# Kernel tuning notes

Measured on AMD Instinct MI355X. Metric: run time of the kernel, lower is better.

The kernel has to match this reference:

```python
import jax, jax.numpy as jnp
import numpy as np
import math

B, L, D, H = 4, 4096, 1024, 16
d = D // H

def setup_inputs() -> dict:
    key = jax.random.key(0)
    ks = jax.random.split(key, 8)
    s = 0.02
    x = jax.random.normal(ks[0], (B, L, D), dtype=jnp.float32)
    Wqkv_w = jax.random.normal(ks[1], (3 * D, D), dtype=jnp.float32) * s
    Wqkv_b = jnp.zeros((3 * D,), dtype=jnp.float32)
    out_w = jax.random.normal(ks[2], (D, D), dtype=jnp.float32) * s
    out_b = jnp.zeros((D,), dtype=jnp.float32)
    W_static = jax.random.normal(ks[3], (H, d, d), dtype=jnp.float32) * s
    Lambda_raw = jax.random.uniform(ks[4], (H, d, d), dtype=jnp.float32, minval=-3.0, maxval=3.0)
    g = 0.5 / math.sqrt(d)
    Gamma = jax.random.uniform(ks[5], (H, d, d), dtype=jnp.float32, minval=-g, maxval=g)
    return {"x": x, "Wqkv_w": Wqkv_w, "Wqkv_b": Wqkv_b, "out_w": out_w,
            "out_b": out_b, "W_static": W_static, "Lambda_raw": Lambda_raw, "Gamma": Gamma}

def _stp_forward(x, Wqkv_w, Wqkv_b, out_w, out_b, W_static, Lambda_raw, Gamma):
    b, l, dm = x.shape
    scale = 1.0 / math.sqrt(d)
    qkv = x @ Wqkv_w.T + Wqkv_b                      # (B,L,3D)
    qkv = qkv.reshape(b, l, 3, H, d)                 # 'b l (three h d)'
    qkv = jnp.transpose(qkv, (2, 0, 3, 1, 4))        # (3,B,H,L,d)
    q, k, v = qkv[0], qkv[1], qkv[2]
    k = k * scale
    retention = 1.0 - jax.nn.sigmoid(Lambda_raw)     # (H,d,d)

    # scan over time: carry state (B,H,d,d)
    qs = jnp.moveaxis(q, 2, 0)                       # (L,B,H,d)
    ks_ = jnp.moveaxis(k, 2, 0)
    vs = jnp.moveaxis(v, 2, 0)

    def step(state, qkv_t):
        q_t, k_t, v_t = qkv_t                        # each (B,H,d)
        hebbian = jnp.einsum('bhi,bhj->bhij', v_t, k_t)
        state = retention[None] * state + Gamma[None] * hebbian
        y_t = jnp.einsum('bhij,bhj->bhi', W_static[None] + state, q_t)
        return state, y_t

    state0 = jnp.zeros((b, H, d, d), dtype=x.dtype)
    _, ys = jax.lax.scan(step, state0, (qs, ks_, vs))  # ys: (L,B,H,d)
    y = jnp.transpose(ys, (1, 0, 2, 3)).reshape(b, l, dm)  # 'b h l d -> b l (h d)'
    return y @ out_w.T + out_b

def reference(x, Wqkv_w, Wqkv_b, out_w, out_b, W_static, Lambda_raw, Gamma):
    return _stp_forward(x, Wqkv_w, Wqkv_b, out_w, out_b, W_static, Lambda_raw, Gamma)
```

## Files before the change

kernel.cpp:

```cpp
#include <hip/hip_runtime.h>
#include <stdint.h>

typedef unsigned short u16;
typedef __bf16 bf16x8 __attribute__((ext_vector_type(8)));
typedef float  f32x4  __attribute__((ext_vector_type(4)));

#define GLOBAL_AS __attribute__((address_space(1)))
#define LDS_AS    __attribute__((address_space(3)))

#define B_ 4
#define L_ 4096
#define D_ 1024
#define H_ 16
#define TD 3072
#define NCHUNK 16
#define TCHUNK 256

__device__ __forceinline__ float bf2f(u16 h) {
    union { uint32_t u; float f; } v; v.u = ((uint32_t)h) << 16; return v.f;
}
__device__ __forceinline__ u16 f2bf(float f) {
    union { float f; uint32_t u; } v; v.f = f;
    uint32_t u = v.u;
    u += 0x7fffu + ((u >> 16) & 1u);
    return (u16)(u >> 16);
}
__device__ __forceinline__ void unp8(uint4 u, float* f) {
    f[0] = bf2f((u16)(u.x)); f[1] = bf2f((u16)(u.x >> 16));
    f[2] = bf2f((u16)(u.y)); f[3] = bf2f((u16)(u.y >> 16));
    f[4] = bf2f((u16)(u.z)); f[5] = bf2f((u16)(u.z >> 16));
    f[6] = bf2f((u16)(u.w)); f[7] = bf2f((u16)(u.w >> 16));
}

__device__ __forceinline__ uint4 ld8f(const float* p) {
    const float4 a = *(const float4*)p;
    const float4 b = *(const float4*)(p + 4);
    uint4 r;
    r.x = (uint32_t)f2bf(a.x) | ((uint32_t)f2bf(a.y) << 16);
    r.y = (uint32_t)f2bf(a.z) | ((uint32_t)f2bf(a.w) << 16);
    r.z = (uint32_t)f2bf(b.x) | ((uint32_t)f2bf(b.y) << 16);
    r.w = (uint32_t)f2bf(b.z) | ((uint32_t)f2bf(b.w) << 16);
    return r;
}

__device__ __forceinline__ void stc(u16* p, float v)   { *p = f2bf(v); }
__device__ __forceinline__ void stc(float* p, float v) { *p = v; }

__global__ __launch_bounds__(256) void cvt_f32_bf16(
    const float* __restrict__ in, u16* __restrict__ out, size_t n8)
{
    size_t i = (size_t)blockIdx.x * 256 + threadIdx.x;
    if (i >= n8) return;
    *(uint4*)(out + i * 8) = ld8f(in + i * 8);
}

template <typename TC>
__global__ __launch_bounds__(256) void gemm_bt_bias_bf16(
    const u16* __restrict__ A, const u16* __restrict__ W,
    const float* __restrict__ bias, TC* __restrict__ C,
    int M, int N, int K)
{
    __shared__ u16 As[128 * 32];
    __shared__ u16 Bs[128 * 32];

    const int tid  = threadIdx.x;
    const int lane = tid & 63;
    const int wid  = tid >> 6;
    const int bm = blockIdx.y * 128;
    const int bn = blockIdx.x * 128;

    const int wm = (wid & 1) * 64;
    const int wn = (wid >> 1) * 64;
    const int fr   = lane & 15;
    const int quad = lane >> 4;

    const u16* Ag = A + (size_t)(bm + (tid >> 2)) * K + (tid & 3) * 8;
    const u16* Wg = W + (size_t)(bn + (tid >> 2)) * K + (tid & 3) * 8;
    const size_t rskip = (size_t)64 * K;

    u16* AsW = As + wid * 512;
    u16* BsW = Bs + wid * 512;

    f32x4 acc[4][4] = {};

    for (int k0 = 0; k0 < K; k0 += 32) {
        __syncthreads();
        __builtin_amdgcn_global_load_lds((const GLOBAL_AS void*)(Ag + k0),
                                         (LDS_AS void*)(AsW),        16, 0, 0);
        __builtin_amdgcn_global_load_lds((const GLOBAL_AS void*)(Ag + rskip + k0),
                                         (LDS_AS void*)(AsW + 2048), 16, 0, 0);
        __builtin_amdgcn_global_load_lds((const GLOBAL_AS void*)(Wg + k0),
                                         (LDS_AS void*)(BsW),        16, 0, 0);
        __builtin_amdgcn_global_load_lds((const GLOBAL_AS void*)(Wg + rskip + k0),
                                         (LDS_AS void*)(BsW + 2048), 16, 0, 0);
        __syncthreads();

        bf16x8 af[4], bfv[4];
#pragma unroll
        for (int tm = 0; tm < 4; ++tm) {
            int m = wm + tm * 16 + fr;
            af[tm] = *(const bf16x8*)&As[m * 32 + quad * 8];
        }
#pragma unroll
        for (int tn = 0; tn < 4; ++tn) {
            int n = wn + tn * 16 + fr;
            bfv[tn] = *(const bf16x8*)&Bs[n * 32 + quad * 8];
        }
#pragma unroll
        for (int tm = 0; tm < 4; ++tm)
#pragma unroll
            for (int tn = 0; tn < 4; ++tn)
                acc[tm][tn] = __builtin_amdgcn_mfma_f32_16x16x32_bf16(
                    af[tm], bfv[tn], acc[tm][tn], 0, 0, 0);
    }

#pragma unroll
    for (int tm = 0; tm < 4; ++tm) {
#pragma unroll
        for (int tn = 0; tn < 4; ++tn) {
            const int col = bn + wn + tn * 16 + fr;
            const float bv = bias[col];
#pragma unroll
            for (int r = 0; r < 4; ++r) {
                const int row = bm + wm + tm * 16 + quad * 4 + r;
                stc(&C[(size_t)row * N + col], acc[tm][tn][r] + bv);
            }
        }
    }
}

__global__ __launch_bounds__(256, 4) void stp_scan_local(
    const u16* __restrict__ qkv, const float* __restrict__ Lam,
    const float* __restrict__ Gam, float* __restrict__ F)
{
    const int c = blockIdx.x, h = blockIdx.y, b = blockIdx.z;
    const int t = threadIdx.x;
    const int ig = t >> 3, jc = t & 7;
    const int i0 = ig << 1, j0 = jc << 3;
    const int hij = (h << 12) + (i0 << 6) + j0;

    float R[2][8], Gv[2][8], s[2][8];
#pragma unroll
    for (int r = 0; r < 2; ++r)
#pragma unroll
        for (int j = 0; j < 8; ++j) {
            R[r][j]  = 1.0f / (1.0f + expf(Lam[hij + r * 64 + j]));
            Gv[r][j] = Gam[hij + r * 64 + j] * 0.125f;
            s[r][j]  = 0.0f;
        }

    const u16* rowp = qkv + (size_t)(b * L_ + c * TCHUNK) * TD;
    const int koff = D_ + (h << 6) + j0;
    const int voff = 2 * D_ + (h << 6) + i0;

    uint4    ku = *(const uint4*)(rowp + koff);
    uint32_t vu = *(const uint32_t*)(rowp + voff);

    for (int tt = 0; tt < TCHUNK; ++tt) {
        uint4    kn = *(const uint4*)(rowp + TD + koff);
        uint32_t vn = *(const uint32_t*)(rowp + TD + voff);

        float kf[8];
        unp8(ku, kf);
        const float v0 = bf2f((u16)vu);
        const float v1 = bf2f((u16)(vu >> 16));
#pragma unroll
        for (int j = 0; j < 8; ++j) {
            s[0][j] = fmaf(R[0][j], s[0][j], (Gv[0][j] * v0) * kf[j]);
            s[1][j] = fmaf(R[1][j], s[1][j], (Gv[1][j] * v1) * kf[j]);
        }
        ku = kn; vu = vn; rowp += TD;
    }

    float* Fp = F + (((size_t)(b * H_ + h) * NCHUNK + c) << 12) + (i0 << 6) + j0;
#pragma unroll
    for (int r = 0; r < 2; ++r) {
        *(f32x4*)(Fp + r * 64)     = *(const f32x4*)(&s[r][0]);
        *(f32x4*)(Fp + r * 64 + 4) = *(const f32x4*)(&s[r][4]);
    }
}

__global__ __launch_bounds__(256) void stp_combine(
    const float* __restrict__ Lam, float* __restrict__ F)
{
    const int h = blockIdx.x, b = blockIdx.y;
    const int t = threadIdx.x;
    const int i = t >> 2, jc = t & 3, j0 = jc << 4;
    const int hij = (h << 12) + (i << 6) + j0;

    float Rt[16], s[16];
#pragma unroll
    for (int j = 0; j < 16; ++j) {
        float R = 1.0f / (1.0f + expf(Lam[hij + j]));
        Rt[j] = powf(R, (float)TCHUNK);
        s[j] = 0.0f;
    }
    float* base = F + (((size_t)(b * H_ + h) * NCHUNK) << 12) + (i << 6) + j0;
    for (int c = 0; c < NCHUNK; ++c) {
        float* p = base + ((size_t)c << 12);
        float tmp[16];
#pragma unroll
        for (int j = 0; j < 16; ++j) tmp[j] = p[j];
#pragma unroll
        for (int j = 0; j < 16; ++j) { p[j] = s[j]; s[j] = fmaf(Rt[j], s[j], tmp[j]); }
    }
}

__global__ __launch_bounds__(256, 4) void stp_scan_out(
    const u16* __restrict__ qkv, const float* __restrict__ Lam,
    const float* __restrict__ Gam, const float* __restrict__ Wst,
    const float* __restrict__ Sinit, u16* __restrict__ y)
{
    const int c = blockIdx.x, h = blockIdx.y, b = blockIdx.z;
    const int t = threadIdx.x;
    const int ig = t >> 3, jc = t & 7;
    const int i0 = ig << 1, j0 = jc << 3;
    const int hij = (h << 12) + (i0 << 6) + j0;

    float R[2][8], Gv[2][8], Cc[2][8], s[2][8];
    const float* Sp = Sinit + (((size_t)(b * H_ + h) * NCHUNK + c) << 12) + (i0 << 6) + j0;
#pragma unroll
    for (int r = 0; r < 2; ++r)
#pragma unroll
        for (int j = 0; j < 8; ++j) {
            const float Rv = 1.0f / (1.0f + expf(Lam[hij + r * 64 + j]));
            const float Wv = Wst[hij + r * 64 + j];
            R[r][j]  = Rv;
            Gv[r][j] = Gam[hij + r * 64 + j] * 0.125f;
            Cc[r][j] = Wv * (1.0f - Rv);
            s[r][j]  = Sp[r * 64 + j] + Wv;
        }

    const u16* rowp = qkv + (size_t)(b * L_ + c * TCHUNK) * TD;
    const int qoff = (h << 6) + j0;
    const int koff = D_ + qoff;
    const int voff = 2 * D_ + (h << 6) + i0;
    u16* yp = y + (size_t)(b * L_ + c * TCHUNK) * D_ + (h << 6) + i0;

    uint4    qu = *(const uint4*)(rowp + qoff);
    uint4    ku = *(const uint4*)(rowp + koff);
    uint32_t vu = *(const uint32_t*)(rowp + voff);

    for (int tt = 0; tt < TCHUNK; ++tt) {
        uint4    qn = *(const uint4*)(rowp + TD + qoff);
        uint4    kn = *(const uint4*)(rowp + TD + koff);
        uint32_t vn = *(const uint32_t*)(rowp + TD + voff);

        float qf[8], kf[8];
        unp8(qu, qf); unp8(ku, kf);
        const float v0 = bf2f((u16)vu);
        const float v1 = bf2f((u16)(vu >> 16));

        float ya0 = 0.0f, ya1 = 0.0f;
#pragma unroll
        for (int j = 0; j < 8; ++j) {
            s[0][j] = fmaf(R[0][j], s[0][j], fmaf(Gv[0][j] * v0, kf[j], Cc[0][j]));
            ya0 = fmaf(s[0][j], qf[j], ya0);
            s[1][j] = fmaf(R[1][j], s[1][j], fmaf(Gv[1][j] * v1, kf[j], Cc[1][j]));
            ya1 = fmaf(s[1][j], qf[j], ya1);
        }
        ya0 += __shfl_xor(ya0, 1, 64);
        ya0 += __shfl_xor(ya0, 2, 64);
        ya0 += __shfl_xor(ya0, 4, 64);
        ya1 += __shfl_xor(ya1, 1, 64);
        ya1 += __shfl_xor(ya1, 2, 64);
        ya1 += __shfl_xor(ya1, 4, 64);
        if (jc == 0) {
            uint32_t pk = (uint32_t)f2bf(ya0) | ((uint32_t)f2bf(ya1) << 16);
            *(uint32_t*)yp = pk;
        }
        qu = qn; ku = kn; vu = vn;
        rowp += TD; yp += D_;
    }
}

__global__ void zero_out_f32(float* p, size_t n) {
    size_t i = (size_t)blockIdx.x * blockDim.x + threadIdx.x;
    if (i < n) p[i] = 0.0f;
}

extern "C" void kernel_launch(void* const* d_in, const int* in_sizes, int n_in,
                              void* d_out, int out_size, void* d_ws, size_t ws_size,
                              hipStream_t stream)
{
    const float* x      = (const float*)d_in[0];
    const float* Wqkv_w = (const float*)d_in[1];
    const float* Wqkv_b = (const float*)d_in[2];
    const float* out_w  = (const float*)d_in[3];
    const float* out_b  = (const float*)d_in[4];
    const float* Wst    = (const float*)d_in[5];
    const float* Lam    = (const float*)d_in[6];
    const float* Gam    = (const float*)d_in[7];
    float* out = (float*)d_out;

    const size_t need = (size_t)B_ * L_ * TD * 2 + (size_t)B_ * L_ * D_ * 2
                      + (size_t)B_ * H_ * NCHUNK * 64 * 64 * 4;
    if (ws_size < need) {
        zero_out_f32<<<(out_size + 255) / 256, 256, 0, stream>>>(out, (size_t)out_size);
        return;
    }
    u16*   qkv = (u16*)d_ws;
    u16*   y   = qkv + (size_t)B_ * L_ * TD;
    float* F   = (float*)(y + (size_t)B_ * L_ * D_);
    u16*   xb    = y;
    u16*   wqkvb = (u16*)F;
    u16*   outwb = (u16*)F;

    cvt_f32_bf16<<<(B_ * L_ * D_ / 8 + 255) / 256, 256, 0, stream>>>(
        x, xb, (size_t)B_ * L_ * D_ / 8);
    cvt_f32_bf16<<<(TD * D_ / 8 + 255) / 256, 256, 0, stream>>>(
        Wqkv_w, wqkvb, (size_t)TD * D_ / 8);
    gemm_bt_bias_bf16<u16><<<dim3(TD / 128, (B_ * L_) / 128), 256, 0, stream>>>(
        xb, wqkvb, Wqkv_b, qkv, B_ * L_, TD, D_);
    stp_scan_local<<<dim3(NCHUNK, H_, B_), 256, 0, stream>>>(qkv, Lam, Gam, F);
    stp_combine<<<dim3(H_, B_), 256, 0, stream>>>(Lam, F);
    stp_scan_out<<<dim3(NCHUNK, H_, B_), 256, 0, stream>>>(qkv, Lam, Gam, Wst, F, y);
    cvt_f32_bf16<<<(D_ * D_ / 8 + 255) / 256, 256, 0, stream>>>(
        out_w, outwb, (size_t)D_ * D_ / 8);
    gemm_bt_bias_bf16<float><<<dim3(D_ / 128, (B_ * L_) / 128), 256, 0, stream>>>(
        y, outwb, out_b, out, B_ * L_, D_, D_);
}
```

Baseline: 670.1 us.

## Split scan blocks over state rows, halving per-thread work, and use DPP row reductions

Each scan block now covers half of the 64 state rows, so the grid doubles and each thread holds a 2x4 slice of the state instead of 2x8. The goal is more parallelism and occupancy in the latency-bound sequential scan over each 256-step chunk. The output-scan reduction across j now runs over 16 lanes using DPP row_shr steps instead of shuffles, and bf16 unpacking uses mask and shift. In exchange, each block loads k, q and v with narrower per-thread loads, and the q/k rows are fetched by twice as many blocks.

```diff
diff --git a/kernel.cpp b/kernel.cpp
--- a/kernel.cpp
+++ b/kernel.cpp
@@ -25,11 +25,28 @@
     u += 0x7fffu + ((u >> 16) & 1u);
     return (u16)(u >> 16);
 }
+__device__ __forceinline__ void unp2(uint32_t u, float* f) {
+    union { uint32_t u; float f; } lo, hi;
+    lo.u = u << 16; hi.u = u & 0xffff0000u;
+    f[0] = lo.f; f[1] = hi.f;
+}
+__device__ __forceinline__ void unp4(uint2 u, float* f) {
+    unp2(u.x, f); unp2(u.y, f + 2);
+}
 __device__ __forceinline__ void unp8(uint4 u, float* f) {
-    f[0] = bf2f((u16)(u.x)); f[1] = bf2f((u16)(u.x >> 16));
-    f[2] = bf2f((u16)(u.y)); f[3] = bf2f((u16)(u.y >> 16));
-    f[4] = bf2f((u16)(u.z)); f[5] = bf2f((u16)(u.z >> 16));
-    f[6] = bf2f((u16)(u.w)); f[7] = bf2f((u16)(u.w >> 16));
+    unp2(u.x, f); unp2(u.y, f + 2); unp2(u.z, f + 4); unp2(u.w, f + 6);
+}
+
+#define DPP_STEP(N)                                                           \
+    {                                                                         \
+        union { float f; int i; } s_, a_;                                     \
+        a_.f = x;                                                             \
+        s_.i = __builtin_amdgcn_update_dpp(0, a_.i, 0x110 + N, 0xf, 0xf, true); \
+        x += s_.f;                                                            \
+    }
+__device__ __forceinline__ float row_sum16(float x) {
+    DPP_STEP(1) DPP_STEP(2) DPP_STEP(4) DPP_STEP(8)
+    return x;
 }
 
 __device__ __forceinline__ uint4 ld8f(const float* p) {
@@ -129,21 +146,22 @@
     }
 }
 
-__global__ __launch_bounds__(256, 4) void stp_scan_local(
+__global__ __launch_bounds__(256, 8) void stp_scan_local(
     const u16* __restrict__ qkv, const float* __restrict__ Lam,
     const float* __restrict__ Gam, float* __restrict__ F)
 {
-    const int c = blockIdx.x, h = blockIdx.y, b = blockIdx.z;
+    const int cx = blockIdx.x, h = blockIdx.y, b = blockIdx.z;
+    const int c = cx >> 1, ih = cx & 1;
     const int t = threadIdx.x;
-    const int ig = t >> 3, jc = t & 7;
-    const int i0 = ig << 1, j0 = jc << 3;
+    const int ig = t >> 4, jc = t & 15;
+    const int i0 = ih * 32 + ig * 2, j0 = jc << 2;
     const int hij = (h << 12) + (i0 << 6) + j0;
 
-    float R[2][8], Gv[2][8], s[2][8];
+    float R[2][4], Gv[2][4], s[2][4];
 #pragma unroll
     for (int r = 0; r < 2; ++r)
 #pragma unroll
-        for (int j = 0; j < 8; ++j) {
+        for (int j = 0; j < 4; ++j) {
             R[r][j]  = 1.0f / (1.0f + expf(Lam[hij + r * 64 + j]));
             Gv[r][j] = Gam[hij + r * 64 + j] * 0.125f;
             s[r][j]  = 0.0f;
@@ -153,19 +171,19 @@
     const int koff = D_ + (h << 6) + j0;
     const int voff = 2 * D_ + (h << 6) + i0;
 
-    uint4    ku = *(const uint4*)(rowp + koff);
+    uint2    ku = *(const uint2*)(rowp + koff);
     uint32_t vu = *(const uint32_t*)(rowp + voff);
 
     for (int tt = 0; tt < TCHUNK; ++tt) {
-        uint4    kn = *(const uint4*)(rowp + TD + koff);
+        uint2    kn = *(const uint2*)(rowp + TD + koff);
         uint32_t vn = *(const uint32_t*)(rowp + TD + voff);
 
-        float kf[8];
-        unp8(ku, kf);
+        float kf[4];
+        unp4(ku, kf);
         const float v0 = bf2f((u16)vu);
         const float v1 = bf2f((u16)(vu >> 16));
 #pragma unroll
-        for (int j = 0; j < 8; ++j) {
+        for (int j = 0; j < 4; ++j) {
             s[0][j] = fmaf(R[0][j], s[0][j], (Gv[0][j] * v0) * kf[j]);
             s[1][j] = fmaf(R[1][j], s[1][j], (Gv[1][j] * v1) * kf[j]);
         }
@@ -173,11 +191,8 @@
     }
 
     float* Fp = F + (((size_t)(b * H_ + h) * NCHUNK + c) << 12) + (i0 << 6) + j0;
-#pragma unroll
-    for (int r = 0; r < 2; ++r) {
-        *(f32x4*)(Fp + r * 64)     = *(const f32x4*)(&s[r][0]);
-        *(f32x4*)(Fp + r * 64 + 4) = *(const f32x4*)(&s[r][4]);
-    }
+    *(f32x4*)(Fp)      = *(const f32x4*)(&s[0][0]);
+    *(f32x4*)(Fp + 64) = *(const f32x4*)(&s[1][0]);
 }
 
 __global__ __launch_bounds__(256) void stp_combine(
@@ -206,23 +221,24 @@
     }
 }
 
-__global__ __launch_bounds__(256, 4) void stp_scan_out(
+__global__ __launch_bounds__(256, 7) void stp_scan_out(
     const u16* __restrict__ qkv, const float* __restrict__ Lam,
     const float* __restrict__ Gam, const float* __restrict__ Wst,
     const float* __restrict__ Sinit, u16* __restrict__ y)
 {
-    const int c = blockIdx.x, h = blockIdx.y, b = blockIdx.z;
+    const int cx = blockIdx.x, h = blockIdx.y, b = blockIdx.z;
+    const int c = cx >> 1, ih = cx & 1;
     const int t = threadIdx.x;
-    const int ig = t >> 3, jc = t & 7;
-    const int i0 = ig << 1, j0 = jc << 3;
+    const int ig = t >> 4, jc = t & 15;
+    const int i0 = ih * 32 + ig * 2, j0 = jc << 2;
     const int hij = (h << 12) + (i0 << 6) + j0;
 
-    float R[2][8], Gv[2][8], Cc[2][8], s[2][8];
+    float R[2][4], Gv[2][4], Cc[2][4], s[2][4];
     const float* Sp = Sinit + (((size_t)(b * H_ + h) * NCHUNK + c) << 12) + (i0 << 6) + j0;
 #pragma unroll
     for (int r = 0; r < 2; ++r)
 #pragma unroll
-        for (int j = 0; j < 8; ++j) {
+        for (int j = 0; j < 4; ++j) {
             const float Rv = 1.0f / (1.0f + expf(Lam[hij + r * 64 + j]));
             const float Wv = Wst[hij + r * 64 + j];
             R[r][j]  = Rv;
@@ -237,35 +253,31 @@
     const int voff = 2 * D_ + (h << 6) + i0;
     u16* yp = y + (size_t)(b * L_ + c * TCHUNK) * D_ + (h << 6) + i0;
 
-    uint4    qu = *(const uint4*)(rowp + qoff);
-    uint4    ku = *(const uint4*)(rowp + koff);
+    uint2    qu = *(const uint2*)(rowp + qoff);
+    uint2    ku = *(const uint2*)(rowp + koff);
     uint32_t vu = *(const uint32_t*)(rowp + voff);
 
     for (int tt = 0; tt < TCHUNK; ++tt) {
-        uint4    qn = *(const uint4*)(rowp + TD + qoff);
-        uint4    kn = *(const uint4*)(rowp + TD + koff);
+        uint2    qn = *(const uint2*)(rowp + TD + qoff);
+        uint2    kn = *(const uint2*)(rowp + TD + koff);
         uint32_t vn = *(const uint32_t*)(rowp + TD + voff);
 
-        float qf[8], kf[8];
-        unp8(qu, qf); unp8(ku, kf);
+        float qf[4], kf[4];
+        unp4(qu, qf); unp4(ku, kf);
         const float v0 = bf2f((u16)vu);
         const float v1 = bf2f((u16)(vu >> 16));
 
         float ya0 = 0.0f, ya1 = 0.0f;
 #pragma unroll
-        for (int j = 0; j < 8; ++j) {
+        for (int j = 0; j < 4; ++j) {
             s[0][j] = fmaf(R[0][j], s[0][j], fmaf(Gv[0][j] * v0, kf[j], Cc[0][j]));
             ya0 = fmaf(s[0][j], qf[j], ya0);
             s[1][j] = fmaf(R[1][j], s[1][j], fmaf(Gv[1][j] * v1, kf[j], Cc[1][j]));
             ya1 = fmaf(s[1][j], qf[j], ya1);
         }
-        ya0 += __shfl_xor(ya0, 1, 64);
-        ya0 += __shfl_xor(ya0, 2, 64);
-        ya0 += __shfl_xor(ya0, 4, 64);
-        ya1 += __shfl_xor(ya1, 1, 64);
-        ya1 += __shfl_xor(ya1, 2, 64);
-        ya1 += __shfl_xor(ya1, 4, 64);
-        if (jc == 0) {
+        ya0 = row_sum16(ya0);
+        ya1 = row_sum16(ya1);
+        if (jc == 15) {
             uint32_t pk = (uint32_t)f2bf(ya0) | ((uint32_t)f2bf(ya1) << 16);
             *(uint32_t*)yp = pk;
         }
@@ -312,9 +324,9 @@
         Wqkv_w, wqkvb, (size_t)TD * D_ / 8);
     gemm_bt_bias_bf16<u16><<<dim3(TD / 128, (B_ * L_) / 128), 256, 0, stream>>>(
         xb, wqkvb, Wqkv_b, qkv, B_ * L_, TD, D_);
-    stp_scan_local<<<dim3(NCHUNK, H_, B_), 256, 0, stream>>>(qkv, Lam, Gam, F);
+    stp_scan_local<<<dim3(NCHUNK * 2, H_, B_), 256, 0, stream>>>(qkv, Lam, Gam, F);
     stp_combine<<<dim3(H_, B_), 256, 0, stream>>>(Lam, F);
-    stp_scan_out<<<dim3(NCHUNK, H_, B_), 256, 0, stream>>>(qkv, Lam, Gam, Wst, F, y);
+    stp_scan_out<<<dim3(NCHUNK * 2, H_, B_), 256, 0, stream>>>(qkv, Lam, Gam, Wst, F, y);
     cvt_f32_bf16<<<(D_ * D_ / 8 + 255) / 256, 256, 0, stream>>>(
         out_w, outwb, (size_t)D_ * D_ / 8);
     gemm_bt_bias_bf16<float><<<dim3(D_ / 128, (B_ * L_) / 128), 256, 0, stream>>>(
```

Measured after the change: 690.4 us. 3.0% more time.
